# Kernel optimization log

Measured on AMD Instinct MI355X. Metric: run time of the kernel, lower is better.

The kernel has to match this reference:

```python
import jax, jax.numpy as jnp
import numpy as np

EMBED_DIM = 1024
NUM_HEADS = 16
HEAD_DIM = EMBED_DIM // NUM_HEADS  # used only for the softmax scale


def setup_inputs() -> dict:
    key = jax.random.key(0)
    k_x, k_wqkv, k_bqkv, k_wo, k_bo = jax.random.split(key, 5)
    bound_qkv = 1.0 / np.sqrt(EMBED_DIM)
    return {
        "x": jax.random.normal(k_x, (4, 2048, EMBED_DIM), dtype=jnp.float32),
        "W_qkv": jax.random.uniform(k_wqkv, (EMBED_DIM, 3 * EMBED_DIM), jnp.float32, -bound_qkv, bound_qkv),
        "b_qkv": jax.random.uniform(k_bqkv, (3 * EMBED_DIM,), jnp.float32, -bound_qkv, bound_qkv),
        "W_out": jax.random.uniform(k_wo, (EMBED_DIM, EMBED_DIM), jnp.float32, -bound_qkv, bound_qkv),
        "b_out": jax.random.uniform(k_bo, (EMBED_DIM,), jnp.float32, -bound_qkv, bound_qkv),
    }


def reference(x, W_qkv, b_qkv, W_out, b_out):
    # fused QKV projection: [B,S,3E]
    qkv = jnp.einsum("bse,ef->bsf", x, W_qkv) + b_qkv
    q, k, v = jnp.split(qkv, 3, axis=-1)  # each [B,S,E]
    scale = 1.0 / jnp.sqrt(jnp.float32(HEAD_DIM))
    # NOTE: no head reshape — attention over full embed_dim, scale uses head_dim
    scores = jnp.einsum("bqe,bke->bqk", q, k) * scale  # [B,S,S]
    attn = jax.nn.softmax(scores, axis=-1)
    context = jnp.einsum("bqk,bke->bqe", attn, v)  # [B,S,E]
    return jnp.einsum("bse,ef->bsf", context, W_out) + b_out
```

## Files before the change

### kernel.cpp

```cpp
#include <hip/hip_runtime.h>

typedef unsigned short u16;
typedef __bf16   bf16x8 __attribute__((ext_vector_type(8)));
typedef float    f32x4  __attribute__((ext_vector_type(4)));
typedef unsigned short u16x4 __attribute__((ext_vector_type(4)));
typedef unsigned short u16x8 __attribute__((ext_vector_type(8)));

__device__ inline float bf2f(u16 u) { return __uint_as_float(((unsigned int)u) << 16); }
__device__ inline u16 f2bf(float f) {
    unsigned int u = __float_as_uint(f);
    u += 0x7FFF + ((u >> 16) & 1);
    return (u16)(u >> 16);
}

__device__ inline void gl2lds16(const u16* g, u16* l) {
    __builtin_amdgcn_global_load_lds(
        (const __attribute__((address_space(1))) void*)g,
        (__attribute__((address_space(3))) void*)l, 16, 0, 0);
}

__device__ inline int self_sniff(const u16* x, int* sflag) {
    const int tid = threadIdx.x;
    if (tid < 64) {
        const unsigned idx = tid * 131072u + 65536u;
        const u16 u = x[idx];
        const int e = (u >> 7) & 0xFF;
        const unsigned long long b = __ballot(e >= 100 && e <= 140);
        if (tid == 0) *sflag = (__popcll(b) >= 48) ? 0 : 1;
    }
    __syncthreads();
    return *sflag;
}

__global__ __launch_bounds__(256)
void prep_wx(const u16* __restrict__ x, u16* __restrict__ xbf,
             const void* __restrict__ Wqkv, u16* __restrict__ WqkvT,
             const void* __restrict__ Wout, u16* __restrict__ WoutT,
             u16* __restrict__ Wvbf,
             const void* __restrict__ bqkv, const void* __restrict__ bout,
             u16* __restrict__ bqkvc, u16* __restrict__ boutc,
             int* __restrict__ flagOut, float* __restrict__ sums)
{
    __shared__ int sflag;
    const int isF32 = self_sniff(x, &sflag);
    if (blockIdx.z == 2) {
        const int flat = blockIdx.y * 129 + blockIdx.x;
        if (flat < 4096) {
            const long i = ((long)flat * 256 + threadIdx.x) * 8;
            if (isF32) {
                f32x4 v0 = *(const f32x4*)((const float*)x + i);
                f32x4 v1 = *(const f32x4*)((const float*)x + i + 4);
                u16x8 o;
                o[0]=f2bf(v0[0]); o[1]=f2bf(v0[1]); o[2]=f2bf(v0[2]); o[3]=f2bf(v0[3]);
                o[4]=f2bf(v1[0]); o[5]=f2bf(v1[1]); o[6]=f2bf(v1[2]); o[7]=f2bf(v1[3]);
                *(u16x8*)(xbf + i) = o;
            } else {
                *(u16x8*)(xbf + i) = *(const u16x8*)(x + i);
            }
        } else if (flat < 4112) {
            const int i = (flat - 4096) * 256 + threadIdx.x;
            if (i < 3072) bqkvc[i] = isF32 ? f2bf(((const float*)bqkv)[i]) : ((const u16*)bqkv)[i];
            else { const int j = i - 3072;
                   boutc[j] = isF32 ? f2bf(((const float*)bout)[j]) : ((const u16*)bout)[j]; }
        } else if (flat == 4112) {
            f32x4 z4 = {0.0f, 0.0f, 0.0f, 0.0f};
#pragma unroll
            for (int q = 0; q < 8; ++q)
                *(f32x4*)&sums[threadIdx.x * 32 + q * 4] = z4;
            if (threadIdx.x == 0) flagOut[0] = isF32;
        }
        return;
    }
    const void* in; u16* out; long inStride, outStride;
    if (blockIdx.z == 0) {
        if (blockIdx.x >= 96) return;
        in = Wqkv; out = WqkvT; inStride = 3072; outStride = 1024;
    } else {
        if (blockIdx.x >= 32) return;
        in = Wout; out = WoutT; inStride = 1024; outStride = 1024;
    }
    __shared__ u16 t[32][36];
    const int tid = threadIdx.x;
    const long r0 = (long)blockIdx.y * 32;
    const long c0 = (long)blockIdx.x * 32;
    const int r  = tid >> 3;
    const int c4 = (tid & 7) * 4;
    const long base = (r0 + r) * inStride + c0 + c4;
    u16x4 v;
    if (isF32) {
        f32x4 f = *(const f32x4*)((const float*)in + base);
        v[0] = f2bf(f[0]); v[1] = f2bf(f[1]); v[2] = f2bf(f[2]); v[3] = f2bf(f[3]);
    } else {
        v = *(const u16x4*)((const u16*)in + base);
    }
    if (blockIdx.z == 0 && c0 >= 2048) {
        *(u16x4*)&Wvbf[(r0 + r) * 1024 + (c0 - 2048) + c4] = v;
        return;
    }
    t[r][c4 + 0] = v[0]; t[r][c4 + 1] = v[1]; t[r][c4 + 2] = v[2]; t[r][c4 + 3] = v[3];
    __syncthreads();
    u16x4 o;
    o[0] = t[c4 + 0][r]; o[1] = t[c4 + 1][r]; o[2] = t[c4 + 2][r]; o[3] = t[c4 + 3][r];
    *(u16x4*)&out[(c0 + r) * outStride + r0 + c4] = o;
}

template <int GM, int GN, int WM, int WN>
__device__ __forceinline__ void kloop(
    const u16* __restrict__ A, const u16* __restrict__ Bt,
    int K, long lda, long ldb, long m0, long n0,
    u16* __restrict__ As, u16* __restrict__ Bs, f32x4 (&acc)[WM][WN])
{
    constexpr int BM = GM * WM * 16;
    constexpr int BN = GN * WN * 16;
    constexpr int IA = BM / 32;
    constexpr int IB = BN / 32;
    const int tid  = threadIdx.x;
    const int lane = tid & 63;
    const int wave = tid >> 6;
    const int sr   = tid >> 3;
    const int qg0  = (tid & 7) ^ (sr & 7);
    const u16* pa[IA]; const u16* pb[IB];
    u16* la[IA]; u16* lb[IB];
#pragma unroll
    for (int i = 0; i < IA; ++i) {
        pa[i] = A + (m0 + i * 32 + sr) * lda + qg0 * 8;
        la[i] = As + (i * 256 + wave * 64) * 8;
    }
#pragma unroll
    for (int i = 0; i < IB; ++i) {
        pb[i] = Bt + (n0 + i * 32 + sr) * ldb + qg0 * 8;
        lb[i] = Bs + (i * 256 + wave * 64) * 8;
    }
    const int wm = (wave / GN) * (WM * 16);
    const int wn = (wave % GN) * (WN * 16);
    const int lr = lane & 15;
    const int hk = lane >> 4;
    int aoff[WM][2], boff[WN][2];
#pragma unroll
    for (int i = 0; i < WM; ++i) {
        const int row = wm + i * 16 + lr, r7 = row & 7;
        aoff[i][0] = row * 64 + ((hk     ^ r7) * 8);
        aoff[i][1] = row * 64 + (((4+hk) ^ r7) * 8);
    }
#pragma unroll
    for (int j = 0; j < WN; ++j) {
        const int row = wn + j * 16 + lr, r7 = row & 7;
        boff[j][0] = row * 64 + ((hk     ^ r7) * 8);
        boff[j][1] = row * 64 + (((4+hk) ^ r7) * 8);
    }
    for (int kt = 0; kt < K; kt += 64) {
#pragma unroll
        for (int i = 0; i < IA; ++i) { gl2lds16(pa[i], la[i]); pa[i] += 64; }
#pragma unroll
        for (int i = 0; i < IB; ++i) { gl2lds16(pb[i], lb[i]); pb[i] += 64; }
        __syncthreads();
#pragma unroll
        for (int ks = 0; ks < 2; ++ks) {
            bf16x8 af[WM], bf[WN];
#pragma unroll
            for (int i = 0; i < WM; ++i) af[i] = *(const bf16x8*)&As[aoff[i][ks]];
#pragma unroll
            for (int j = 0; j < WN; ++j) bf[j] = *(const bf16x8*)&Bs[boff[j][ks]];
#pragma unroll
            for (int i = 0; i < WM; ++i)
#pragma unroll
                for (int j = 0; j < WN; ++j)
                    acc[i][j] = __builtin_amdgcn_mfma_f32_16x16x32_bf16(af[i], bf[j], acc[i][j], 0, 0, 0);
        }
        __syncthreads();
    }
}

template <int WM, int WN, typename F>
__device__ __forceinline__ void epi_bf16(u16* __restrict__ Sw, u16* __restrict__ C,
    long ldc, long gm0, long gn0, int lane, F f)
{
    const int lr = lane & 15, hk = lane >> 4;
#pragma unroll
    for (int i = 0; i < WM; ++i)
#pragma unroll
        for (int j = 0; j < WN; ++j)
#pragma unroll
            for (int r = 0; r < 4; ++r)
                Sw[(i*16 + hk*4 + r) * (WN*16) + j*16 + lr] = f2bf(f(i, j, r));
    asm volatile("s_waitcnt lgkmcnt(0)" ::: "memory");
    constexpr int LPR = WN * 2;
    constexpr int RPI = 64 / LPR;
    const int rl = lane / LPR, c8 = (lane % LPR) * 8;
#pragma unroll
    for (int t = 0; t < (WM*16) / RPI; ++t) {
        const int row = t * RPI + rl;
        u16x8 v8 = *(const u16x8*)&Sw[row * (WN*16) + c8];
        *(u16x8*)&C[(gm0 + row) * ldc + gn0 + c8] = v8;
    }
}

template <int WM, int WN, typename F>
__device__ __forceinline__ void epi_f32(float* __restrict__ Sw, float* __restrict__ C,
    long ldc, long gm0, long gn0, int lane, F f)
{
    const int lr = lane & 15, hk = lane >> 4;
#pragma unroll
    for (int jh = 0; jh < 2; ++jh) {
#pragma unroll
        for (int i = 0; i < WM; ++i)
#pragma unroll
            for (int jj = 0; jj < WN/2; ++jj)
#pragma unroll
                for (int r = 0; r < 4; ++r)
                    Sw[(i*16 + hk*4 + r) * (WN*8) + jj*16 + lr] = f(i, jh*(WN/2) + jj, r);
        asm volatile("s_waitcnt lgkmcnt(0)" ::: "memory");
        constexpr int LPR = WN * 2;
        constexpr int RPI = 64 / LPR;
        const int rl = lane / LPR, c4 = (lane % LPR) * 4;
#pragma unroll
        for (int t = 0; t < (WM*16) / RPI; ++t) {
            const int row = t * RPI + rl;
            f32x4 v4 = *(const f32x4*)&Sw[row * (WN*8) + c4];
            *(f32x4*)&C[(gm0 + row) * ldc + gn0 + jh*(WN*8) + c4] = v4;
        }
        asm volatile("s_waitcnt lgkmcnt(0)" ::: "memory");
    }
}

__device__ __forceinline__ void epiT_vw(u16* __restrict__ Sw, u16* __restrict__ VWTb,
    long o0, long t0, int lane, const f32x4 (&acc)[4][4])
{
    const int lr = lane & 15, hk = lane >> 4;
#pragma unroll
    for (int jh = 0; jh < 2; ++jh) {
#pragma unroll
        for (int jj = 0; jj < 2; ++jj) {
            const int j = jh*2 + jj;
            const int fl = jj*16 + lr;
#pragma unroll
            for (int i = 0; i < 4; ++i)
#pragma unroll
                for (int r = 0; r < 4; ++r)
                    Sw[fl*72 + i*16 + hk*4 + r] = f2bf(acc[i][j][r]);
        }
        asm volatile("s_waitcnt lgkmcnt(0)" ::: "memory");
        const int rl = lane >> 3, c8 = (lane & 7) * 8;
#pragma unroll
        for (int s = 0; s < 4; ++s) {
            const int fl = s*8 + rl;
            *(u16x8*)&VWTb[(o0 + jh*32 + fl) * 2048 + t0 + c8] =
                *(const u16x8*)&Sw[fl*72 + c8];
        }
        asm volatile("s_waitcnt lgkmcnt(0)" ::: "memory");
    }
}

__global__ __launch_bounds__(256, 4)
void gemm_qkv(const u16* __restrict__ A, const u16* __restrict__ Bt,
              u16* __restrict__ C, u16* __restrict__ VWT,
              const u16* __restrict__ bias)
{
    __shared__ __align__(16) u16 S[256 * 64];
    const long m0 = (long)blockIdx.y * 128, n0 = (long)blockIdx.x * 128;
    f32x4 acc[4][4] = {};
    kloop<2, 2, 4, 4>(A, Bt, 1024, 1024L, 1024L, m0, n0, S, S + 128*64, acc);
    const int lane = threadIdx.x & 63, wave = threadIdx.x >> 6;
    const int wm = (wave >> 1) * 64, wn = (wave & 1) * 64;
    u16* Sw = S + wave * 4096;
    if (n0 >= 2048) {
        u16* VWTb = VWT + (m0 >> 11) * 1024 * 2048;
        epiT_vw(Sw, VWTb, n0 + wn - 2048, (m0 & 2047) + wm, lane, acc);
    } else {
        const int lr = lane & 15;
        float bj[4];
#pragma unroll
        for (int j = 0; j < 4; ++j) bj[j] = bf2f(bias[n0 + wn + j*16 + lr]);
        epi_bf16<4, 4>(Sw, C, 3072L, m0 + wm, n0 + wn, lane,
            [&](int i, int j, int r) { return acc[i][j][r] + bj[j]; });
    }
}

__global__ __launch_bounds__(256, 4)
void gemm_wvo(const u16* __restrict__ WoutT, const u16* __restrict__ Wvbf,
              u16* __restrict__ WvoT, const u16* __restrict__ bqkvc,
              const u16* __restrict__ boutc, u16* __restrict__ bfinal)
{
    __shared__ __align__(16) u16 S[8192];
    if (blockIdx.x == 16) {
        if (blockIdx.y >= 4) return;
        const int o = blockIdx.y * 256 + threadIdx.x;
        const u16* row = WoutT + (long)o * 1024;
        float s0 = 0, s1 = 0, s2 = 0, s3 = 0, s4 = 0, s5 = 0, s6 = 0, s7 = 0;
        for (int v = 0; v < 1024; v += 8) {
            u16x8 w = *(const u16x8*)&row[v];
            u16x8 b = *(const u16x8*)&bqkvc[2048 + v];
            s0 += bf2f(w[0]) * bf2f(b[0]); s1 += bf2f(w[1]) * bf2f(b[1]);
            s2 += bf2f(w[2]) * bf2f(b[2]); s3 += bf2f(w[3]) * bf2f(b[3]);
            s4 += bf2f(w[4]) * bf2f(b[4]); s5 += bf2f(w[5]) * bf2f(b[5]);
            s6 += bf2f(w[6]) * bf2f(b[6]); s7 += bf2f(w[7]) * bf2f(b[7]);
        }
        const float s = ((s0 + s1) + (s2 + s3)) + ((s4 + s5) + (s6 + s7));
        bfinal[o] = f2bf(s + bf2f(boutc[o]));
        return;
    }
    const long m0 = (long)blockIdx.y * 64, n0 = (long)blockIdx.x * 64;
    f32x4 acc[2][2] = {};
    kloop<2, 2, 2, 2>(WoutT, Wvbf, 1024, 1024L, 1024L, m0, n0, S, S + 4096, acc);
    const int lane = threadIdx.x & 63, wave = threadIdx.x >> 6;
    const int wm = (wave >> 1) * 32, wn = (wave & 1) * 32;
    epi_bf16<2, 2>(S + wave * 1024, WvoT, 1024L, m0 + wm, n0 + wn, lane,
        [&](int i, int j, int r) { return acc[i][j][r]; });
}

__global__ __launch_bounds__(256, 4)
void gemm_scores128(const u16* __restrict__ QKV, u16* __restrict__ P,
                    float* __restrict__ sums)
{
    __shared__ __align__(16) u16 S[256 * 64];
    const int z = blockIdx.z;
    const long zb = (long)z * 2048 * 3072;
    const u16* Ap = QKV + zb;
    const u16* Bp = QKV + 1024 + zb;
    u16* Cp = P + (long)z * 2048 * 2048;
    float* srow = sums + z * 2048;
    const long m0 = (long)blockIdx.y * 128, n0 = (long)blockIdx.x * 128;
    f32x4 acc[4][4] = {};
    kloop<2, 2, 4, 4>(Ap, Bp, 1024, 3072L, 3072L, m0, n0, S, S + 128*64, acc);
    const int lane = threadIdx.x & 63, wave = threadIdx.x >> 6;
    const int wm = (wave >> 1) * 64, wn = (wave & 1) * 64;
    const int lr = lane & 15, hk = lane >> 4;
    u16* Sw = S + wave * 4096;
#pragma unroll
    for (int i = 0; i < 4; ++i)
#pragma unroll
        for (int r = 0; r < 4; ++r) {
            const int lrow = i*16 + hk*4 + r;
            float s = 0.0f;
#pragma unroll
            for (int j = 0; j < 4; ++j) {
                const float e = __expf(acc[i][j][r] * 0.125f);
                Sw[lrow * 64 + j*16 + lr] = f2bf(e);
                s += e;
            }
            s += __shfl_xor(s, 1); s += __shfl_xor(s, 2);
            s += __shfl_xor(s, 4); s += __shfl_xor(s, 8);
            if (lr == 0) atomicAdd(&srow[m0 + wm + lrow], s);
        }
    asm volatile("s_waitcnt lgkmcnt(0)" ::: "memory");
    const int rl = lane >> 3, c8 = (lane & 7) * 8;
#pragma unroll
    for (int t = 0; t < 8; ++t) {
        const int row = t * 8 + rl;
        u16x8 v8 = *(const u16x8*)&Sw[row * 64 + c8];
        *(u16x8*)&Cp[(m0 + wm + row) * 2048 + n0 + wn + c8] = v8;
    }
}

__global__ __launch_bounds__(256, 4)
void gemm_final(const u16* __restrict__ P, const u16* __restrict__ VWT,
                void* __restrict__ out, const u16* __restrict__ bias,
                const float* __restrict__ sums, const int* __restrict__ flagp)
{
    __shared__ __align__(16) u16 S[256 * 64];
    const int outF32 = *flagp;
    const int wg = blockIdx.x + (blockIdx.y << 3) + (blockIdx.z << 7);
    const int f8 = (wg & 7) * 64 + (wg >> 3);
    const long bz = f8 >> 7;
    const long m0 = (long)((f8 >> 3) & 15) * 128, n0 = (long)(f8 & 7) * 128;
    f32x4 acc[4][4] = {};
    kloop<2, 2, 4, 4>(P + bz * 2048 * 2048, VWT + bz * 1024 * 2048,
                      2048, 2048L, 2048L, m0, n0, S, S + 128*64, acc);
    const int lane = threadIdx.x & 63, wave = threadIdx.x >> 6;
    const int wm = (wave >> 1) * 64, wn = (wave & 1) * 64;
    const int lr = lane & 15, hk = lane >> 4;
    float inv[4][4], bj[4];
#pragma unroll
    for (int i = 0; i < 4; ++i)
#pragma unroll
        for (int r = 0; r < 4; ++r)
            inv[i][r] = 1.0f / sums[bz * 2048 + m0 + wm + i*16 + hk*4 + r];
#pragma unroll
    for (int j = 0; j < 4; ++j) bj[j] = bf2f(bias[n0 + wn + j*16 + lr]);
    if (outF32) {
        float* Co = (float*)out + bz * 2048 * 1024;
        epi_f32<4, 4>((float*)S + wave * 2048, Co, 1024L, m0 + wm, n0 + wn, lane,
            [&](int i, int j, int r) { return acc[i][j][r] * inv[i][r] + bj[j]; });
    } else {
        u16* Co = (u16*)out + bz * 2048 * 1024;
        epi_bf16<4, 4>(S + wave * 4096, Co, 1024L, m0 + wm, n0 + wn, lane,
            [&](int i, int j, int r) { return acc[i][j][r] * inv[i][r] + bj[j]; });
    }
}

extern "C" void kernel_launch(void* const* d_in, const int* in_sizes, int n_in,
                              void* d_out, int out_size, void* d_ws, size_t ws_size,
                              hipStream_t stream)
{
    const void* x    = d_in[0];
    const void* Wqkv = d_in[1];
    const void* bqkv = d_in[2];
    const void* Wout = d_in[3];
    const void* bout = d_in[4];
    char* ws = (char*)d_ws;

    u16*   xbf   = (u16*)(ws);
    u16*   WqkvT = (u16*)(ws + 16777216);
    u16*   P     = (u16*)(ws);
    u16*   QKV   = (u16*)(ws + 33554432);
    u16*   VWT   = (u16*)(ws + 83886080);
    u16*   Wvbf  = (u16*)(ws + 83886080);
    u16*   WoutT = (u16*)(ws + 100663296);
    u16*   bqkvc = (u16*)(ws + 102760448);
    u16*   boutc = (u16*)(ws + 102766592);
    int*   flag  = (int*)(ws + 102768640);
    u16*   bfin  = (u16*)(ws + 102769664);
    float* sums  = (float*)(ws + 102772736);

    dim3 blk(256);

    prep_wx<<<dim3(129, 32, 3), blk, 0, stream>>>((const u16*)x, xbf, Wqkv, WqkvT,
                                                  Wout, WoutT, Wvbf, bqkv, bout,
                                                  bqkvc, boutc, flag, sums);

    gemm_wvo<<<dim3(17, 16, 1), blk, 0, stream>>>(WoutT, Wvbf, WqkvT + 2048*1024,
                                                  bqkvc, boutc, bfin);

    gemm_qkv<<<dim3(24, 64, 1), blk, 0, stream>>>(xbf, WqkvT, QKV, VWT, bqkvc);

    gemm_scores128<<<dim3(16, 16, 4), blk, 0, stream>>>(QKV, P, sums);

    gemm_final<<<dim3(8, 16, 4), blk, 0, stream>>>(P, VWT, d_out, bfin, sums, flag);
}
```

Before: 258.3 us.

## Merge all stages into one persistent cooperative kernel with grid syncs

Replaces the five separate kernel launches (prep, Wv·Wo fold, QKV GEMM, scores, final GEMM) with a single persistent cooperative kernel. Each stage loops over tiles across a grid sized from occupancy, and grid.sync() separates the stages. The goal is to cut launch gaps and per-kernel ramp-up and tail costs. In exchange, the grid is capped at 1024 blocks, stage work is spread with strided loops, the tile-to-block mapping may change locality, and every stage must wait at a grid-wide barrier.

```diff
diff --git a/kernel.cpp b/kernel.cpp
--- a/kernel.cpp
+++ b/kernel.cpp
@@ -1,4 +1,7 @@
 #include <hip/hip_runtime.h>
+#include <hip/hip_cooperative_groups.h>
+
+namespace cg = cooperative_groups;
 
 typedef unsigned short u16;
 typedef __bf16   bf16x8 __attribute__((ext_vector_type(8)));
@@ -30,78 +33,6 @@
     }
     __syncthreads();
     return *sflag;
-}
-
-__global__ __launch_bounds__(256)
-void prep_wx(const u16* __restrict__ x, u16* __restrict__ xbf,
-             const void* __restrict__ Wqkv, u16* __restrict__ WqkvT,
-             const void* __restrict__ Wout, u16* __restrict__ WoutT,
-             u16* __restrict__ Wvbf,
-             const void* __restrict__ bqkv, const void* __restrict__ bout,
-             u16* __restrict__ bqkvc, u16* __restrict__ boutc,
-             int* __restrict__ flagOut, float* __restrict__ sums)
-{
-    __shared__ int sflag;
-    const int isF32 = self_sniff(x, &sflag);
-    if (blockIdx.z == 2) {
-        const int flat = blockIdx.y * 129 + blockIdx.x;
-        if (flat < 4096) {
-            const long i = ((long)flat * 256 + threadIdx.x) * 8;
-            if (isF32) {
-                f32x4 v0 = *(const f32x4*)((const float*)x + i);
-                f32x4 v1 = *(const f32x4*)((const float*)x + i + 4);
-                u16x8 o;
-                o[0]=f2bf(v0[0]); o[1]=f2bf(v0[1]); o[2]=f2bf(v0[2]); o[3]=f2bf(v0[3]);
-                o[4]=f2bf(v1[0]); o[5]=f2bf(v1[1]); o[6]=f2bf(v1[2]); o[7]=f2bf(v1[3]);
-                *(u16x8*)(xbf + i) = o;
-            } else {
-                *(u16x8*)(xbf + i) = *(const u16x8*)(x + i);
-            }
-        } else if (flat < 4112) {
-            const int i = (flat - 4096) * 256 + threadIdx.x;
-            if (i < 3072) bqkvc[i] = isF32 ? f2bf(((const float*)bqkv)[i]) : ((const u16*)bqkv)[i];
-            else { const int j = i - 3072;
-                   boutc[j] = isF32 ? f2bf(((const float*)bout)[j]) : ((const u16*)bout)[j]; }
-        } else if (flat == 4112) {
-            f32x4 z4 = {0.0f, 0.0f, 0.0f, 0.0f};
-#pragma unroll
-            for (int q = 0; q < 8; ++q)
-                *(f32x4*)&sums[threadIdx.x * 32 + q * 4] = z4;
-            if (threadIdx.x == 0) flagOut[0] = isF32;
-        }
-        return;
-    }
-    const void* in; u16* out; long inStride, outStride;
-    if (blockIdx.z == 0) {
-        if (blockIdx.x >= 96) return;
-        in = Wqkv; out = WqkvT; inStride = 3072; outStride = 1024;
-    } else {
-        if (blockIdx.x >= 32) return;
-        in = Wout; out = WoutT; inStride = 1024; outStride = 1024;
-    }
-    __shared__ u16 t[32][36];
-    const int tid = threadIdx.x;
-    const long r0 = (long)blockIdx.y * 32;
-    const long c0 = (long)blockIdx.x * 32;
-    const int r  = tid >> 3;
-    const int c4 = (tid & 7) * 4;
-    const long base = (r0 + r) * inStride + c0 + c4;
-    u16x4 v;
-    if (isF32) {
-        f32x4 f = *(const f32x4*)((const float*)in + base);
-        v[0] = f2bf(f[0]); v[1] = f2bf(f[1]); v[2] = f2bf(f[2]); v[3] = f2bf(f[3]);
-    } else {
-        v = *(const u16x4*)((const u16*)in + base);
-    }
-    if (blockIdx.z == 0 && c0 >= 2048) {
-        *(u16x4*)&Wvbf[(r0 + r) * 1024 + (c0 - 2048) + c4] = v;
-        return;
-    }
-    t[r][c4 + 0] = v[0]; t[r][c4 + 1] = v[1]; t[r][c4 + 2] = v[2]; t[r][c4 + 3] = v[3];
-    __syncthreads();
-    u16x4 o;
-    o[0] = t[c4 + 0][r]; o[1] = t[c4 + 1][r]; o[2] = t[c4 + 2][r]; o[3] = t[c4 + 3][r];
-    *(u16x4*)&out[(c0 + r) * outStride + r0 + c4] = o;
 }
 
 template <int GM, int GN, int WM, int WN>
@@ -252,139 +183,203 @@
 }
 
 __global__ __launch_bounds__(256, 4)
-void gemm_qkv(const u16* __restrict__ A, const u16* __restrict__ Bt,
-              u16* __restrict__ C, u16* __restrict__ VWT,
-              const u16* __restrict__ bias)
-{
-    __shared__ __align__(16) u16 S[256 * 64];
-    const long m0 = (long)blockIdx.y * 128, n0 = (long)blockIdx.x * 128;
-    f32x4 acc[4][4] = {};
-    kloop<2, 2, 4, 4>(A, Bt, 1024, 1024L, 1024L, m0, n0, S, S + 128*64, acc);
-    const int lane = threadIdx.x & 63, wave = threadIdx.x >> 6;
-    const int wm = (wave >> 1) * 64, wn = (wave & 1) * 64;
-    u16* Sw = S + wave * 4096;
-    if (n0 >= 2048) {
-        u16* VWTb = VWT + (m0 >> 11) * 1024 * 2048;
-        epiT_vw(Sw, VWTb, n0 + wn - 2048, (m0 & 2047) + wm, lane, acc);
-    } else {
-        const int lr = lane & 15;
-        float bj[4];
-#pragma unroll
-        for (int j = 0; j < 4; ++j) bj[j] = bf2f(bias[n0 + wn + j*16 + lr]);
-        epi_bf16<4, 4>(Sw, C, 3072L, m0 + wm, n0 + wn, lane,
-            [&](int i, int j, int r) { return acc[i][j][r] + bj[j]; });
-    }
-}
-
-__global__ __launch_bounds__(256, 4)
-void gemm_wvo(const u16* __restrict__ WoutT, const u16* __restrict__ Wvbf,
-              u16* __restrict__ WvoT, const u16* __restrict__ bqkvc,
-              const u16* __restrict__ boutc, u16* __restrict__ bfinal)
-{
-    __shared__ __align__(16) u16 S[8192];
-    if (blockIdx.x == 16) {
-        if (blockIdx.y >= 4) return;
-        const int o = blockIdx.y * 256 + threadIdx.x;
-        const u16* row = WoutT + (long)o * 1024;
-        float s0 = 0, s1 = 0, s2 = 0, s3 = 0, s4 = 0, s5 = 0, s6 = 0, s7 = 0;
-        for (int v = 0; v < 1024; v += 8) {
-            u16x8 w = *(const u16x8*)&row[v];
-            u16x8 b = *(const u16x8*)&bqkvc[2048 + v];
-            s0 += bf2f(w[0]) * bf2f(b[0]); s1 += bf2f(w[1]) * bf2f(b[1]);
-            s2 += bf2f(w[2]) * bf2f(b[2]); s3 += bf2f(w[3]) * bf2f(b[3]);
-            s4 += bf2f(w[4]) * bf2f(b[4]); s5 += bf2f(w[5]) * bf2f(b[5]);
-            s6 += bf2f(w[6]) * bf2f(b[6]); s7 += bf2f(w[7]) * bf2f(b[7]);
-        }
-        const float s = ((s0 + s1) + (s2 + s3)) + ((s4 + s5) + (s6 + s7));
-        bfinal[o] = f2bf(s + bf2f(boutc[o]));
-        return;
-    }
-    const long m0 = (long)blockIdx.y * 64, n0 = (long)blockIdx.x * 64;
-    f32x4 acc[2][2] = {};
-    kloop<2, 2, 2, 2>(WoutT, Wvbf, 1024, 1024L, 1024L, m0, n0, S, S + 4096, acc);
-    const int lane = threadIdx.x & 63, wave = threadIdx.x >> 6;
-    const int wm = (wave >> 1) * 32, wn = (wave & 1) * 32;
-    epi_bf16<2, 2>(S + wave * 1024, WvoT, 1024L, m0 + wm, n0 + wn, lane,
-        [&](int i, int j, int r) { return acc[i][j][r]; });
-}
-
-__global__ __launch_bounds__(256, 4)
-void gemm_scores128(const u16* __restrict__ QKV, u16* __restrict__ P,
-                    float* __restrict__ sums)
-{
-    __shared__ __align__(16) u16 S[256 * 64];
-    const int z = blockIdx.z;
-    const long zb = (long)z * 2048 * 3072;
-    const u16* Ap = QKV + zb;
-    const u16* Bp = QKV + 1024 + zb;
-    u16* Cp = P + (long)z * 2048 * 2048;
-    float* srow = sums + z * 2048;
-    const long m0 = (long)blockIdx.y * 128, n0 = (long)blockIdx.x * 128;
-    f32x4 acc[4][4] = {};
-    kloop<2, 2, 4, 4>(Ap, Bp, 1024, 3072L, 3072L, m0, n0, S, S + 128*64, acc);
-    const int lane = threadIdx.x & 63, wave = threadIdx.x >> 6;
-    const int wm = (wave >> 1) * 64, wn = (wave & 1) * 64;
-    const int lr = lane & 15, hk = lane >> 4;
-    u16* Sw = S + wave * 4096;
-#pragma unroll
-    for (int i = 0; i < 4; ++i)
-#pragma unroll
-        for (int r = 0; r < 4; ++r) {
-            const int lrow = i*16 + hk*4 + r;
-            float s = 0.0f;
-#pragma unroll
-            for (int j = 0; j < 4; ++j) {
-                const float e = __expf(acc[i][j][r] * 0.125f);
-                Sw[lrow * 64 + j*16 + lr] = f2bf(e);
-                s += e;
-            }
-            s += __shfl_xor(s, 1); s += __shfl_xor(s, 2);
-            s += __shfl_xor(s, 4); s += __shfl_xor(s, 8);
-            if (lr == 0) atomicAdd(&srow[m0 + wm + lrow], s);
-        }
-    asm volatile("s_waitcnt lgkmcnt(0)" ::: "memory");
-    const int rl = lane >> 3, c8 = (lane & 7) * 8;
-#pragma unroll
-    for (int t = 0; t < 8; ++t) {
-        const int row = t * 8 + rl;
-        u16x8 v8 = *(const u16x8*)&Sw[row * 64 + c8];
-        *(u16x8*)&Cp[(m0 + wm + row) * 2048 + n0 + wn + c8] = v8;
-    }
-}
-
-__global__ __launch_bounds__(256, 4)
-void gemm_final(const u16* __restrict__ P, const u16* __restrict__ VWT,
-                void* __restrict__ out, const u16* __restrict__ bias,
-                const float* __restrict__ sums, const int* __restrict__ flagp)
-{
-    __shared__ __align__(16) u16 S[256 * 64];
-    const int outF32 = *flagp;
-    const int wg = blockIdx.x + (blockIdx.y << 3) + (blockIdx.z << 7);
-    const int f8 = (wg & 7) * 64 + (wg >> 3);
-    const long bz = f8 >> 7;
-    const long m0 = (long)((f8 >> 3) & 15) * 128, n0 = (long)(f8 & 7) * 128;
-    f32x4 acc[4][4] = {};
-    kloop<2, 2, 4, 4>(P + bz * 2048 * 2048, VWT + bz * 1024 * 2048,
-                      2048, 2048L, 2048L, m0, n0, S, S + 128*64, acc);
-    const int lane = threadIdx.x & 63, wave = threadIdx.x >> 6;
-    const int wm = (wave >> 1) * 64, wn = (wave & 1) * 64;
-    const int lr = lane & 15, hk = lane >> 4;
-    float inv[4][4], bj[4];
-#pragma unroll
-    for (int i = 0; i < 4; ++i)
-#pragma unroll
-        for (int r = 0; r < 4; ++r)
-            inv[i][r] = 1.0f / sums[bz * 2048 + m0 + wm + i*16 + hk*4 + r];
-#pragma unroll
-    for (int j = 0; j < 4; ++j) bj[j] = bf2f(bias[n0 + wn + j*16 + lr]);
-    if (outF32) {
-        float* Co = (float*)out + bz * 2048 * 1024;
-        epi_f32<4, 4>((float*)S + wave * 2048, Co, 1024L, m0 + wm, n0 + wn, lane,
-            [&](int i, int j, int r) { return acc[i][j][r] * inv[i][r] + bj[j]; });
-    } else {
-        u16* Co = (u16*)out + bz * 2048 * 1024;
-        epi_bf16<4, 4>(S + wave * 4096, Co, 1024L, m0 + wm, n0 + wn, lane,
-            [&](int i, int j, int r) { return acc[i][j][r] * inv[i][r] + bj[j]; });
+void mega(const u16* __restrict__ x, u16* xbf,
+          const void* __restrict__ Wqkv, u16* WqkvT,
+          const void* __restrict__ Wout, u16* WoutT,
+          u16* Wvbf,
+          const void* __restrict__ bqkv, const void* __restrict__ bout,
+          u16* __restrict__ bqkvc, u16* __restrict__ boutc,
+          float* __restrict__ sums, u16* WvoT,
+          u16* __restrict__ bfin, u16* QKV,
+          u16* VWT, u16* P, void* __restrict__ out)
+{
+    __shared__ __align__(16) u16 S[16384];
+    const int tid = threadIdx.x;
+    const unsigned bid = blockIdx.x;
+    const unsigned gsz = gridDim.x;
+    cg::grid_group grid = cg::this_grid();
+
+    const int isF32 = self_sniff(x, (int*)S);
+    __syncthreads();
+
+    for (unsigned t = bid; t < 8209; t += gsz) {
+        __syncthreads();
+        if (t < 4096) {
+            const long i = ((long)t * 256 + tid) * 8;
+            if (isF32) {
+                f32x4 v0 = *(const f32x4*)((const float*)x + i);
+                f32x4 v1 = *(const f32x4*)((const float*)x + i + 4);
+                u16x8 o;
+                o[0]=f2bf(v0[0]); o[1]=f2bf(v0[1]); o[2]=f2bf(v0[2]); o[3]=f2bf(v0[3]);
+                o[4]=f2bf(v1[0]); o[5]=f2bf(v1[1]); o[6]=f2bf(v1[2]); o[7]=f2bf(v1[3]);
+                *(u16x8*)(xbf + i) = o;
+            } else {
+                *(u16x8*)(xbf + i) = *(const u16x8*)(x + i);
+            }
+        } else if (t < 8192) {
+            const int isWq = (t < 7168);
+            const void* in; u16* outp; long inStride, outStride, r0, c0;
+            if (isWq) {
+                const unsigned u = t - 4096;
+                in = Wqkv; outp = WqkvT; inStride = 3072; outStride = 1024;
+                c0 = (long)(u % 96) * 32; r0 = (long)(u / 96) * 32;
+            } else {
+                const unsigned u = t - 7168;
+                in = Wout; outp = WoutT; inStride = 1024; outStride = 1024;
+                c0 = (long)(u & 31) * 32; r0 = (long)(u >> 5) * 32;
+            }
+            u16 (*tt)[36] = (u16(*)[36])S;
+            const int r = tid >> 3, c4 = (tid & 7) * 4;
+            const long base = (r0 + r) * inStride + c0 + c4;
+            u16x4 v;
+            if (isF32) {
+                f32x4 f = *(const f32x4*)((const float*)in + base);
+                v[0]=f2bf(f[0]); v[1]=f2bf(f[1]); v[2]=f2bf(f[2]); v[3]=f2bf(f[3]);
+            } else {
+                v = *(const u16x4*)((const u16*)in + base);
+            }
+            if (isWq && c0 >= 2048) {
+                *(u16x4*)&Wvbf[(r0 + r) * 1024 + (c0 - 2048) + c4] = v;
+            } else {
+                tt[r][c4+0]=v[0]; tt[r][c4+1]=v[1]; tt[r][c4+2]=v[2]; tt[r][c4+3]=v[3];
+                __syncthreads();
+                u16x4 o;
+                o[0]=tt[c4+0][r]; o[1]=tt[c4+1][r]; o[2]=tt[c4+2][r]; o[3]=tt[c4+3][r];
+                *(u16x4*)&outp[(c0 + r) * outStride + r0 + c4] = o;
+            }
+        } else if (t < 8208) {
+            const int i = (int)(t - 8192) * 256 + tid;
+            if (i < 3072) bqkvc[i] = isF32 ? f2bf(((const float*)bqkv)[i]) : ((const u16*)bqkv)[i];
+            else { const int j = i - 3072;
+                   boutc[j] = isF32 ? f2bf(((const float*)bout)[j]) : ((const u16*)bout)[j]; }
+        } else {
+            f32x4 z4 = {0.0f, 0.0f, 0.0f, 0.0f};
+#pragma unroll
+            for (int q = 0; q < 8; ++q) *(f32x4*)&sums[tid * 32 + q * 4] = z4;
+        }
+    }
+    grid.sync();
+
+    for (unsigned t = bid; t < 260; t += gsz) {
+        __syncthreads();
+        if (t < 256) {
+            const long m0 = (long)(t >> 4) * 64, n0 = (long)(t & 15) * 64;
+            f32x4 acc[2][2] = {};
+            kloop<2, 2, 2, 2>(WoutT, Wvbf, 1024, 1024L, 1024L, m0, n0, S, S + 4096, acc);
+            const int lane = tid & 63, wave = tid >> 6;
+            const int wm = (wave >> 1) * 32, wn = (wave & 1) * 32;
+            epi_bf16<2, 2>(S + wave * 1024, WvoT, 1024L, m0 + wm, n0 + wn, lane,
+                [&](int i, int j, int r) { return acc[i][j][r]; });
+        } else {
+            const int o = (int)(t - 256) * 256 + tid;
+            const u16* row = WoutT + (long)o * 1024;
+            float s0=0,s1=0,s2=0,s3=0,s4=0,s5=0,s6=0,s7=0;
+            for (int v = 0; v < 1024; v += 8) {
+                u16x8 w = *(const u16x8*)&row[v];
+                u16x8 b = *(const u16x8*)&bqkvc[2048 + v];
+                s0 += bf2f(w[0])*bf2f(b[0]); s1 += bf2f(w[1])*bf2f(b[1]);
+                s2 += bf2f(w[2])*bf2f(b[2]); s3 += bf2f(w[3])*bf2f(b[3]);
+                s4 += bf2f(w[4])*bf2f(b[4]); s5 += bf2f(w[5])*bf2f(b[5]);
+                s6 += bf2f(w[6])*bf2f(b[6]); s7 += bf2f(w[7])*bf2f(b[7]);
+            }
+            const float s = ((s0+s1)+(s2+s3)) + ((s4+s5)+(s6+s7));
+            bfin[o] = f2bf(s + bf2f(boutc[o]));
+        }
+    }
+    grid.sync();
+
+    for (unsigned t = bid; t < 1536; t += gsz) {
+        __syncthreads();
+        const long m0 = (long)(t / 24) * 128, n0 = (long)(t % 24) * 128;
+        f32x4 acc[4][4] = {};
+        kloop<2, 2, 4, 4>(xbf, WqkvT, 1024, 1024L, 1024L, m0, n0, S, S + 8192, acc);
+        const int lane = tid & 63, wave = tid >> 6;
+        const int wm = (wave >> 1) * 64, wn = (wave & 1) * 64;
+        u16* Sw = S + wave * 4096;
+        if (n0 >= 2048) {
+            u16* VWTb = VWT + (m0 >> 11) * 1024 * 2048;
+            epiT_vw(Sw, VWTb, n0 + wn - 2048, (m0 & 2047) + wm, lane, acc);
+        } else {
+            const int lr = lane & 15;
+            float bj[4];
+#pragma unroll
+            for (int j = 0; j < 4; ++j) bj[j] = bf2f(bqkvc[n0 + wn + j*16 + lr]);
+            epi_bf16<4, 4>(Sw, QKV, 3072L, m0 + wm, n0 + wn, lane,
+                [&](int i, int j, int r) { return acc[i][j][r] + bj[j]; });
+        }
+    }
+    grid.sync();
+
+    for (unsigned t = bid; t < 1024; t += gsz) {
+        __syncthreads();
+        const int z = (int)(t >> 8);
+        const long m0 = (long)((t >> 4) & 15) * 128, n0 = (long)(t & 15) * 128;
+        const long zb = (long)z * 2048 * 3072;
+        const u16* Ap = QKV + zb;
+        const u16* Bp = QKV + 1024 + zb;
+        u16* Cp = P + (long)z * 2048 * 2048;
+        float* srow = sums + z * 2048;
+        f32x4 acc[4][4] = {};
+        kloop<2, 2, 4, 4>(Ap, Bp, 1024, 3072L, 3072L, m0, n0, S, S + 8192, acc);
+        const int lane = tid & 63, wave = tid >> 6;
+        const int wm = (wave >> 1) * 64, wn = (wave & 1) * 64;
+        const int lr = lane & 15, hk = lane >> 4;
+        u16* Sw = S + wave * 4096;
+#pragma unroll
+        for (int i = 0; i < 4; ++i)
+#pragma unroll
+            for (int r = 0; r < 4; ++r) {
+                const int lrow = i*16 + hk*4 + r;
+                float s = 0.0f;
+#pragma unroll
+                for (int j = 0; j < 4; ++j) {
+                    const float e = __expf(acc[i][j][r] * 0.125f);
+                    Sw[lrow * 64 + j*16 + lr] = f2bf(e);
+                    s += e;
+                }
+                s += __shfl_xor(s, 1); s += __shfl_xor(s, 2);
+                s += __shfl_xor(s, 4); s += __shfl_xor(s, 8);
+                if (lr == 0) atomicAdd(&srow[m0 + wm + lrow], s);
+            }
+        asm volatile("s_waitcnt lgkmcnt(0)" ::: "memory");
+        const int rl = lane >> 3, c8 = (lane & 7) * 8;
+#pragma unroll
+        for (int q = 0; q < 8; ++q) {
+            const int row = q * 8 + rl;
+            u16x8 v8 = *(const u16x8*)&Sw[row * 64 + c8];
+            *(u16x8*)&Cp[(m0 + wm + row) * 2048 + n0 + wn + c8] = v8;
+        }
+    }
+    grid.sync();
+
+    for (unsigned t = bid; t < 512; t += gsz) {
+        __syncthreads();
+        const int f8 = (int)((t & 7) * 64 + (t >> 3));
+        const long bz = f8 >> 7;
+        const long m0 = (long)((f8 >> 3) & 15) * 128, n0 = (long)(f8 & 7) * 128;
+        f32x4 acc[4][4] = {};
+        kloop<2, 2, 4, 4>(P + bz * 2048 * 2048, VWT + bz * 1024 * 2048,
+                          2048, 2048L, 2048L, m0, n0, S, S + 8192, acc);
+        const int lane = tid & 63, wave = tid >> 6;
+        const int wm = (wave >> 1) * 64, wn = (wave & 1) * 64;
+        const int lr = lane & 15, hk = lane >> 4;
+        float inv[4][4], bj[4];
+#pragma unroll
+        for (int i = 0; i < 4; ++i)
+#pragma unroll
+            for (int r = 0; r < 4; ++r)
+                inv[i][r] = 1.0f / sums[bz * 2048 + m0 + wm + i*16 + hk*4 + r];
+#pragma unroll
+        for (int j = 0; j < 4; ++j) bj[j] = bf2f(bfin[n0 + wn + j*16 + lr]);
+        if (isF32) {
+            float* Co = (float*)out + bz * 2048 * 1024;
+            epi_f32<4, 4>((float*)S + wave * 2048, Co, 1024L, m0 + wm, n0 + wn, lane,
+                [&](int i, int j, int r) { return acc[i][j][r] * inv[i][r] + bj[j]; });
+        } else {
+            u16* Co = (u16*)out + bz * 2048 * 1024;
+            epi_bf16<4, 4>(S + wave * 4096, Co, 1024L, m0 + wm, n0 + wn, lane,
+                [&](int i, int j, int r) { return acc[i][j][r] * inv[i][r] + bj[j]; });
+        }
     }
 }
 
@@ -392,7 +387,7 @@
                               void* d_out, int out_size, void* d_ws, size_t ws_size,
                               hipStream_t stream)
 {
-    const void* x    = d_in[0];
+    const u16* x     = (const u16*)d_in[0];
     const void* Wqkv = d_in[1];
     const void* bqkv = d_in[2];
     const void* Wout = d_in[3];
@@ -408,22 +403,27 @@
     u16*   WoutT = (u16*)(ws + 100663296);
     u16*   bqkvc = (u16*)(ws + 102760448);
     u16*   boutc = (u16*)(ws + 102766592);
-    int*   flag  = (int*)(ws + 102768640);
     u16*   bfin  = (u16*)(ws + 102769664);
     float* sums  = (float*)(ws + 102772736);
-
-    dim3 blk(256);
-
-    prep_wx<<<dim3(129, 32, 3), blk, 0, stream>>>((const u16*)x, xbf, Wqkv, WqkvT,
-                                                  Wout, WoutT, Wvbf, bqkv, bout,
-                                                  bqkvc, boutc, flag, sums);
-
-    gemm_wvo<<<dim3(17, 16, 1), blk, 0, stream>>>(WoutT, Wvbf, WqkvT + 2048*1024,
-                                                  bqkvc, boutc, bfin);
-
-    gemm_qkv<<<dim3(24, 64, 1), blk, 0, stream>>>(xbf, WqkvT, QKV, VWT, bqkvc);
-
-    gemm_scores128<<<dim3(16, 16, 4), blk, 0, stream>>>(QKV, P, sums);
-
-    gemm_final<<<dim3(8, 16, 4), blk, 0, stream>>>(P, VWT, d_out, bfin, sums, flag);
-}
+    u16*   WvoT  = WqkvT + 2048 * 1024;
+
+    static int gridN = 0;
+    if (gridN == 0) {
+        int maxB = 0;
+        hipOccupancyMaxActiveBlocksPerMultiprocessor(&maxB, (const void*)mega, 256, 0);
+        hipDeviceProp_t prop;
+        hipGetDeviceProperties(&prop, 0);
+        long cap = (long)maxB * prop.multiProcessorCount;
+        gridN = (int)(cap < 1024 ? cap : 1024);
+        if (gridN < 8) gridN = 8;
+    }
+
+    void* args[] = {
+        (void*)&x, (void*)&xbf, (void*)&Wqkv, (void*)&WqkvT, (void*)&Wout,
+        (void*)&WoutT, (void*)&Wvbf, (void*)&bqkv, (void*)&bout, (void*)&bqkvc,
+        (void*)&boutc, (void*)&sums, (void*)&WvoT, (void*)&bfin, (void*)&QKV,
+        (void*)&VWT, (void*)&P, (void*)&d_out
+    };
+    hipLaunchCooperativeKernel((const void*)mega, dim3(gridN), dim3(256),
+                               args, 0, stream);
+}
```

Measured after the change: 574.1 us. 122% more time.
